# Kernel tuning notes

Hardware: AMD Instinct MI355X
Metric: run time of the kernel (lower is better)

Reference implementation:

```python
import jax, jax.numpy as jnp
import numpy as np

N_NODES = 50000
FEAT_DIM = 256
HIDDEN = 64
CLASS_DIM = 64
N_EDGES = 800000
K_HOPS = 2


def setup_inputs() -> dict:
    key = jax.random.key(0)
    k1, k2, k3, k4, k5, k6 = jax.random.split(key, 6)
    x = jax.random.normal(k1, (N_NODES, FEAT_DIM), dtype=jnp.float32)
    edge_rows = jax.random.randint(k2, (N_EDGES,), 0, N_NODES, dtype=jnp.int32)
    edge_cols = jax.random.randint(k3, (N_EDGES,), 0, N_NODES, dtype=jnp.int32)
    edge_vals = jax.random.uniform(k4, (N_EDGES,), dtype=jnp.float32)  # normalized-adj values (>0)
    # xavier_uniform-style init scale
    lim_e = float(np.sqrt(6.0 / (FEAT_DIM + HIDDEN)))
    lim_c = float(np.sqrt(6.0 / (7 * HIDDEN + CLASS_DIM)))
    w_embed = jax.random.uniform(k5, (FEAT_DIM, HIDDEN), dtype=jnp.float32, minval=-lim_e, maxval=lim_e)
    w_classify = jax.random.uniform(k6, (7 * HIDDEN, CLASS_DIM), dtype=jnp.float32, minval=-lim_c, maxval=lim_c)
    return {"x": x, "edge_rows": edge_rows, "edge_cols": edge_cols,
            "edge_vals": edge_vals, "w_embed": w_embed, "w_classify": w_classify}


def reference(x, edge_rows, edge_cols, edge_vals, w_embed, w_classify):
    # Node_GCN forward (eval mode; dropout inert).
    # a1 = adj - I, a2 = adj@adj - adj - I  =>
    #   a1 @ r = s - r,   a2 @ r = adj@s - s - r   with s = adj @ r
    n = x.shape[0]

    def spmm(r):  # adj @ r via edge-list gather + segment-sum: [n, d]
        return jax.ops.segment_sum(edge_vals[:, None] * r[edge_cols], edge_rows, num_segments=n)

    act = jax.nn.relu
    r = act(x @ w_embed)                  # [n, h]
    rs = [r]
    for _ in range(K_HOPS):
        s = spmm(r)                       # adj @ r
        t = spmm(s)                       # adj @ adj @ r
        r1 = s - r                        # a1 @ r
        r2 = t - s - r                    # a2 @ r
        r = act(jnp.concatenate([r1, r2], axis=1))  # width doubles each hop
        rs.append(r)
    r_final = jnp.concatenate(rs, axis=1)  # [n, 7h]
    return jax.nn.softmax(r_final @ w_classify, axis=1)
```

## Files before the change

kernel.cpp:

```cpp
#include <hip/hip_runtime.h>

#define N_NODES 50000
#define NPAD 50048
#define FEAT 256
#define HID 64
#define NEDGE 800000
#define SCAN_CHUNK 2048
#define NB_SCAN 25
#define NB_EDGE 3125
#define NB_GEMM 391

typedef unsigned short bf16_t;
typedef __attribute__((ext_vector_type(8))) short bf16x8;
typedef __attribute__((ext_vector_type(4))) float f32x4;

#define MFMA_BF16 __builtin_amdgcn_mfma_f32_16x16x32_bf16

__device__ __forceinline__ float bf2f(bf16_t b) {
    union { unsigned u; float f; } v; v.u = ((unsigned)b) << 16; return v.f;
}
__device__ __forceinline__ bf16_t f2bf(float f) {
    union { float f; unsigned u; } v; v.f = f;
    unsigned r = v.u + 0x7fff + ((v.u >> 16) & 1);
    return (bf16_t)(r >> 16);
}
__device__ __forceinline__ void unpack2(unsigned u, float& lo, float& hi) {
    union { unsigned u; float f; } a, b;
    a.u = u << 16; b.u = u & 0xffff0000u;
    lo = a.f; hi = b.f;
}
__device__ __forceinline__ unsigned pack2(float lo, float hi) {
    return ((unsigned)f2bf(lo)) | (((unsigned)f2bf(hi)) << 16);
}

__device__ __forceinline__ void pack_w_body(const float* __restrict__ wsrc,
        bf16_t* __restrict__ wdst, int idx) {
    int lane = idx & 63, nt = (idx >> 6) & 3, ks = idx >> 8;
    int kb  = ks * 32 + ((lane >> 4) * 8);
    int col = nt * 16 + (lane & 15);
    unsigned p[4];
#pragma unroll
    for (int j = 0; j < 4; ++j)
        p[j] = pack2(wsrc[(size_t)(kb + 2*j) * 64 + col],
                     wsrc[(size_t)(kb + 2*j + 1) * 64 + col]);
    uint4 u; u.x = p[0]; u.y = p[1]; u.z = p[2]; u.w = p[3];
    *(uint4*)(wdst + (size_t)idx * 8) = u;
}

__global__ __launch_bounds__(256) void prep_kernel(const int* __restrict__ rows,
        int* __restrict__ cnt, const float* __restrict__ we, bf16_t* __restrict__ wep,
        const float* __restrict__ wc, bf16_t* __restrict__ wcp) {
    const int b = blockIdx.x, t = threadIdx.x;
    if (b < NB_EDGE) {
        int e = b * 256 + t;
        if (e < NEDGE) atomicAdd(&cnt[rows[e]], 1);
    } else if (b < NB_EDGE + 8) {
        pack_w_body(we, wep, (b - NB_EDGE) * 256 + t);
    } else {
        pack_w_body(wc, wcp, (b - NB_EDGE - 8) * 256 + t);
    }
}

__global__ __launch_bounds__(256) void scan_a(const int* __restrict__ cnt,
        int* __restrict__ bsum) {
    __shared__ int sd[256];
    const int t = threadIdx.x;
    const int base = blockIdx.x * SCAN_CHUNK + t * 8;
    int s = 0;
#pragma unroll
    for (int i = 0; i < 8; ++i) {
        int idx = base + i;
        s += (idx < N_NODES) ? cnt[idx] : 0;
    }
    sd[t] = s; __syncthreads();
    for (int off = 128; off > 0; off >>= 1) {
        if (t < off) sd[t] += sd[t + off];
        __syncthreads();
    }
    if (t == 0) bsum[blockIdx.x] = sd[0];
}

__global__ __launch_bounds__(256) void scan_c(const int* __restrict__ cnt,
        const int* __restrict__ bsum, int* __restrict__ rowPtr,
        int* __restrict__ fill) {
    __shared__ int sd[256];
    __shared__ int sboff;
    const int t = threadIdx.x;
    const int base = blockIdx.x * SCAN_CHUNK + t * 8;
    if (t == 0) {
        int a = 0, tot = 0;
        for (int b = 0; b < NB_SCAN; ++b) {
            int v = bsum[b];
            if (b < (int)blockIdx.x) a += v;
            tot += v;
        }
        sboff = a;
        if (blockIdx.x == NB_SCAN - 1) rowPtr[N_NODES] = tot;
    }
    int v[8];
    int s = 0;
#pragma unroll
    for (int i = 0; i < 8; ++i) {
        int idx = base + i;
        v[i] = (idx < N_NODES) ? cnt[idx] : 0;
        s += v[i];
    }
    sd[t] = s; __syncthreads();
    for (int off = 1; off < 256; off <<= 1) {
        int add = (t >= off) ? sd[t - off] : 0;
        __syncthreads();
        sd[t] += add;
        __syncthreads();
    }
    int run = sboff + (sd[t] - s);
#pragma unroll
    for (int i = 0; i < 8; ++i) {
        int idx = base + i;
        if (idx < N_NODES) { rowPtr[idx] = run; fill[idx] = 0; }
        run += v[i];
    }
}

__global__ __launch_bounds__(256) void scatter_embed_kernel(
        const int* __restrict__ rows, const int* __restrict__ cols,
        const float* __restrict__ vals, const int* __restrict__ rowPtr,
        int* __restrict__ fill, uint2* __restrict__ colval,
        const float* __restrict__ x, const bf16_t* __restrict__ wep,
        bf16_t* __restrict__ r0) {
    if (blockIdx.x < NB_EDGE) {
        int e = blockIdx.x * 256 + threadIdx.x;
        if (e < NEDGE) {
            int r = rows[e];
            int p = rowPtr[r] + atomicAdd(&fill[r], 1);
            uint2 cv; cv.x = (unsigned)cols[e]; cv.y = __float_as_uint(vals[e]);
            colval[p] = cv;
        }
        return;
    }
    const int blk = blockIdx.x - NB_EDGE;
    const int t = threadIdx.x;
    const int l = t & 63, w = t >> 6;
    const int lm = l & 15, lg = l >> 4;
    const int base = blk * 128 + w * 32;

    int m0 = base + lm, m1 = base + 16 + lm;
    if (m0 >= N_NODES) m0 = N_NODES - 1;
    if (m1 >= N_NODES) m1 = N_NODES - 1;
    const float* xp0 = x + (size_t)m0 * FEAT + lg * 8;
    const float* xp1 = x + (size_t)m1 * FEAT + lg * 8;

    f32x4 acc[2][4];
#pragma unroll
    for (int i = 0; i < 2; ++i)
#pragma unroll
        for (int j = 0; j < 4; ++j) acc[i][j] = (f32x4){0.f, 0.f, 0.f, 0.f};

    auto aload = [&](const float* p) {
        float4 u0 = *(const float4*)(p);
        float4 u1 = *(const float4*)(p + 4);
        bf16x8 r;
        r[0] = (short)f2bf(u0.x); r[1] = (short)f2bf(u0.y);
        r[2] = (short)f2bf(u0.z); r[3] = (short)f2bf(u0.w);
        r[4] = (short)f2bf(u1.x); r[5] = (short)f2bf(u1.y);
        r[6] = (short)f2bf(u1.z); r[7] = (short)f2bf(u1.w);
        return r;
    };
    auto wb = [&](int ks, int nt) {
        return *(const bf16x8*)(wep + ((size_t)(ks * 4 + nt) * 64 + l) * 8);
    };

    const int NK = FEAT / 32;
    bf16x8 a0 = aload(xp0), a1 = aload(xp1);
    bf16x8 b0 = wb(0,0), b1 = wb(0,1), b2 = wb(0,2), b3 = wb(0,3);
    for (int ks = 0; ks < NK; ++ks) {
        bf16x8 na0, na1, nb0, nb1, nb2, nb3;
        const bool more = (ks + 1 < NK);
        if (more) {
            int kt = (ks + 1) * 32;
            na0 = aload(xp0 + kt); na1 = aload(xp1 + kt);
            nb0 = wb(ks+1,0); nb1 = wb(ks+1,1); nb2 = wb(ks+1,2); nb3 = wb(ks+1,3);
        }
        acc[0][0] = MFMA_BF16(a0, b0, acc[0][0], 0, 0, 0);
        acc[1][0] = MFMA_BF16(a1, b0, acc[1][0], 0, 0, 0);
        acc[0][1] = MFMA_BF16(a0, b1, acc[0][1], 0, 0, 0);
        acc[1][1] = MFMA_BF16(a1, b1, acc[1][1], 0, 0, 0);
        acc[0][2] = MFMA_BF16(a0, b2, acc[0][2], 0, 0, 0);
        acc[1][2] = MFMA_BF16(a1, b2, acc[1][2], 0, 0, 0);
        acc[0][3] = MFMA_BF16(a0, b3, acc[0][3], 0, 0, 0);
        acc[1][3] = MFMA_BF16(a1, b3, acc[1][3], 0, 0, 0);
        if (more) { a0 = na0; a1 = na1; b0 = nb0; b1 = nb1; b2 = nb2; b3 = nb3; }
    }

#pragma unroll
    for (int rt = 0; rt < 2; ++rt)
#pragma unroll
        for (int r = 0; r < 4; ++r) {
            int R = base + rt * 16 + lg * 4 + r;
            if (R < N_NODES) {
                bf16_t* o = r0 + (size_t)R * HID + lm;
                o[0]  = f2bf(fmaxf(acc[rt][0][r], 0.f));
                o[16] = f2bf(fmaxf(acc[rt][1][r], 0.f));
                o[32] = f2bf(fmaxf(acc[rt][2][r], 0.f));
                o[48] = f2bf(fmaxf(acc[rt][3][r], 0.f));
            }
        }
}

__global__ __launch_bounds__(256) void spmm64_kernel(const uint2* __restrict__ colval,
        const int* __restrict__ rowPtr,
        const bf16_t* __restrict__ src, bf16_t* __restrict__ dst) {
    const int lane = threadIdx.x & 63;
    const int row  = (int)((blockIdx.x * 256u + threadIdx.x) >> 6);
    const int beg = rowPtr[row], end = rowPtr[row + 1];
    float acc = 0.f;
    int i = beg;
    for (; i + 8 <= end; i += 8) {
        uint2 cv[8]; float g[8];
#pragma unroll
        for (int j = 0; j < 8; ++j) cv[j] = colval[i+j];
#pragma unroll
        for (int j = 0; j < 8; ++j) g[j] = bf2f(src[(size_t)cv[j].x*HID + lane]);
#pragma unroll
        for (int j = 0; j < 8; ++j) acc += __uint_as_float(cv[j].y)*g[j];
    }
    for (; i < end; ++i) {
        uint2 cv = colval[i];
        acc += __uint_as_float(cv.y) * bf2f(src[(size_t)cv.x*HID + lane]);
    }
    dst[(size_t)row*HID + lane] = f2bf(acc);
}

__global__ __launch_bounds__(256) void spmm64f_kernel(const uint2* __restrict__ colval,
        const int* __restrict__ rowPtr,
        const bf16_t* __restrict__ s, const bf16_t* __restrict__ r0,
        bf16_t* __restrict__ r1c) {
    const int lane = threadIdx.x & 63;
    const int row  = (int)((blockIdx.x * 256u + threadIdx.x) >> 6);
    const int beg = rowPtr[row], end = rowPtr[row + 1];
    float acc = 0.f;
    int i = beg;
    for (; i + 8 <= end; i += 8) {
        uint2 cv[8]; float g[8];
#pragma unroll
        for (int j = 0; j < 8; ++j) cv[j] = colval[i+j];
#pragma unroll
        for (int j = 0; j < 8; ++j) g[j] = bf2f(s[(size_t)cv[j].x*HID + lane]);
#pragma unroll
        for (int j = 0; j < 8; ++j) acc += __uint_as_float(cv[j].y)*g[j];
    }
    for (; i < end; ++i) {
        uint2 cv = colval[i];
        acc += __uint_as_float(cv.y) * bf2f(s[(size_t)cv.x*HID + lane]);
    }
    float sv = bf2f(s[(size_t)row*HID + lane]);
    float rv = bf2f(r0[(size_t)row*HID + lane]);
    r1c[(size_t)row*128 + lane]      = f2bf(fmaxf(sv - rv, 0.f));
    r1c[(size_t)row*128 + 64 + lane] = f2bf(fmaxf(acc - sv - rv, 0.f));
}

__global__ __launch_bounds__(256) void spmm128_kernel(const uint2* __restrict__ colval,
        const int* __restrict__ rowPtr,
        const bf16_t* __restrict__ src, bf16_t* __restrict__ dst) {
    const int lane = threadIdx.x & 63;
    const int row  = (int)((blockIdx.x * 256u + threadIdx.x) >> 6);
    const int beg = rowPtr[row], end = rowPtr[row + 1];
    const unsigned* srcu = (const unsigned*)src;
    float a0 = 0.f, a1 = 0.f;
    int i = beg;
    for (; i + 4 <= end; i += 4) {
        uint2 cv[4]; unsigned u[4];
#pragma unroll
        for (int j = 0; j < 4; ++j) cv[j] = colval[i+j];
#pragma unroll
        for (int j = 0; j < 4; ++j) u[j] = srcu[(size_t)cv[j].x*64 + lane];
#pragma unroll
        for (int j = 0; j < 4; ++j) {
            float lo, hi; unpack2(u[j], lo, hi);
            float v = __uint_as_float(cv[j].y);
            a0 += v*lo; a1 += v*hi;
        }
    }
    for (; i < end; ++i) {
        uint2 cv = colval[i];
        float lo, hi; unpack2(srcu[(size_t)cv.x*64 + lane], lo, hi);
        float v = __uint_as_float(cv.y);
        a0 += v*lo; a1 += v*hi;
    }
    ((unsigned*)dst)[(size_t)row*64 + lane] = pack2(a0, a1);
}

__global__ __launch_bounds__(256) void spmm128f_kernel(const uint2* __restrict__ colval,
        const int* __restrict__ rowPtr,
        const bf16_t* __restrict__ s2, const bf16_t* __restrict__ r1,
        bf16_t* __restrict__ r2c) {
    const int lane = threadIdx.x & 63;
    const int row  = (int)((blockIdx.x * 256u + threadIdx.x) >> 6);
    const int beg = rowPtr[row], end = rowPtr[row + 1];
    const unsigned* s2u = (const unsigned*)s2;
    const unsigned* r1u = (const unsigned*)r1;
    float a0 = 0.f, a1 = 0.f;
    int i = beg;
    for (; i + 4 <= end; i += 4) {
        uint2 cv[4]; unsigned u[4];
#pragma unroll
        for (int j = 0; j < 4; ++j) cv[j] = colval[i+j];
#pragma unroll
        for (int j = 0; j < 4; ++j) u[j] = s2u[(size_t)cv[j].x*64 + lane];
#pragma unroll
        for (int j = 0; j < 4; ++j) {
            float lo, hi; unpack2(u[j], lo, hi);
            float v = __uint_as_float(cv[j].y);
            a0 += v*lo; a1 += v*hi;
        }
    }
    for (; i < end; ++i) {
        uint2 cv = colval[i];
        float lo, hi; unpack2(s2u[(size_t)cv.x*64 + lane], lo, hi);
        float v = __uint_as_float(cv.y);
        a0 += v*lo; a1 += v*hi;
    }
    float s0v, s1v, r0v, r1v;
    unpack2(s2u[(size_t)row*64 + lane], s0v, s1v);
    unpack2(r1u[(size_t)row*64 + lane], r0v, r1v);
    unsigned* r2u = (unsigned*)r2c;
    r2u[(size_t)row*128 + lane]      = pack2(fmaxf(s0v - r0v, 0.f), fmaxf(s1v - r1v, 0.f));
    r2u[(size_t)row*128 + 64 + lane] = pack2(fmaxf(a0 - s0v - r0v, 0.f), fmaxf(a1 - s1v - r1v, 0.f));
}

__global__ __launch_bounds__(256) void classify_mfma(const bf16_t* __restrict__ r0,
        const bf16_t* __restrict__ r1, const bf16_t* __restrict__ r2,
        const bf16_t* __restrict__ wcp, float* __restrict__ out) {
    const int t = threadIdx.x;
    const int l = t & 63, w = t >> 6;
    const int lm = l & 15, lg = l >> 4;
    const int base = blockIdx.x * 128 + w * 32;

    const int m0 = base + lm, m1 = base + 16 + lm;
    const bf16_t* p0_r0 = r0 + (size_t)m0 * 64  + lg * 8;
    const bf16_t* p0_r1 = r1 + (size_t)m0 * 128 + lg * 8;
    const bf16_t* p0_r2 = r2 + (size_t)m0 * 256 + lg * 8;
    const bf16_t* p1_r0 = r0 + (size_t)m1 * 64  + lg * 8;
    const bf16_t* p1_r1 = r1 + (size_t)m1 * 128 + lg * 8;
    const bf16_t* p1_r2 = r2 + (size_t)m1 * 256 + lg * 8;

    f32x4 acc[2][4];
#pragma unroll
    for (int i = 0; i < 2; ++i)
#pragma unroll
        for (int j = 0; j < 4; ++j) acc[i][j] = (f32x4){0.f, 0.f, 0.f, 0.f};

    auto aload = [&](const bf16_t* pr0, const bf16_t* pr1, const bf16_t* pr2, int kt) {
        const bf16_t* p = (kt < 64) ? (pr0 + kt) : (kt < 192) ? (pr1 + kt - 64) : (pr2 + kt - 192);
        return *(const bf16x8*)p;
    };
    auto wb = [&](int ks, int nt) {
        return *(const bf16x8*)(wcp + ((size_t)(ks * 4 + nt) * 64 + l) * 8);
    };

    const int NK = 14;
    bf16x8 a0 = aload(p0_r0, p0_r1, p0_r2, 0);
    bf16x8 a1 = aload(p1_r0, p1_r1, p1_r2, 0);
    bf16x8 b0 = wb(0,0), b1 = wb(0,1), b2 = wb(0,2), b3 = wb(0,3);
    for (int ks = 0; ks < NK; ++ks) {
        bf16x8 na0, na1, nb0, nb1, nb2, nb3;
        const bool more = (ks + 1 < NK);
        if (more) {
            int kt = (ks + 1) * 32;
            na0 = aload(p0_r0, p0_r1, p0_r2, kt);
            na1 = aload(p1_r0, p1_r1, p1_r2, kt);
            nb0 = wb(ks+1,0); nb1 = wb(ks+1,1); nb2 = wb(ks+1,2); nb3 = wb(ks+1,3);
        }
        acc[0][0] = MFMA_BF16(a0, b0, acc[0][0], 0, 0, 0);
        acc[1][0] = MFMA_BF16(a1, b0, acc[1][0], 0, 0, 0);
        acc[0][1] = MFMA_BF16(a0, b1, acc[0][1], 0, 0, 0);
        acc[1][1] = MFMA_BF16(a1, b1, acc[1][1], 0, 0, 0);
        acc[0][2] = MFMA_BF16(a0, b2, acc[0][2], 0, 0, 0);
        acc[1][2] = MFMA_BF16(a1, b2, acc[1][2], 0, 0, 0);
        acc[0][3] = MFMA_BF16(a0, b3, acc[0][3], 0, 0, 0);
        acc[1][3] = MFMA_BF16(a1, b3, acc[1][3], 0, 0, 0);
        if (more) { a0 = na0; a1 = na1; b0 = nb0; b1 = nb1; b2 = nb2; b3 = nb3; }
    }

#pragma unroll
    for (int rt = 0; rt < 2; ++rt)
#pragma unroll
        for (int r = 0; r < 4; ++r) {
            float v0 = acc[rt][0][r], v1 = acc[rt][1][r];
            float v2 = acc[rt][2][r], v3 = acc[rt][3][r];
            float m = fmaxf(fmaxf(v0, v1), fmaxf(v2, v3));
#pragma unroll
            for (int o = 1; o < 16; o <<= 1) m = fmaxf(m, __shfl_xor(m, o));
            float e0 = __expf(v0 - m), e1 = __expf(v1 - m);
            float e2 = __expf(v2 - m), e3 = __expf(v3 - m);
            float s = e0 + e1 + e2 + e3;
#pragma unroll
            for (int o = 1; o < 16; o <<= 1) s += __shfl_xor(s, o);
            float inv = 1.f / s;
            int R = base + rt * 16 + lg * 4 + r;
            if (R < N_NODES) {
                float* o = out + (size_t)R * 64 + lm;
                o[0]  = e0 * inv;
                o[16] = e1 * inv;
                o[32] = e2 * inv;
                o[48] = e3 * inv;
            }
        }
}

extern "C" void kernel_launch(void* const* d_in, const int* in_sizes, int n_in,
                              void* d_out, int out_size, void* d_ws, size_t ws_size,
                              hipStream_t stream) {
    const float* x    = (const float*)d_in[0];
    const int*   erow = (const int*)d_in[1];
    const int*   ecol = (const int*)d_in[2];
    const float* eval = (const float*)d_in[3];
    const float* we   = (const float*)d_in[4];
    const float* wc   = (const float*)d_in[5];
    float* out = (float*)d_out;

    char* wsp = (char*)d_ws;
    size_t off = 0;
    auto take = [&](size_t bytes) {
        char* p = wsp + off;
        off += (bytes + 255) & ~(size_t)255;
        return p;
    };
    bf16_t* r0     = (bf16_t*)take((size_t)NPAD * 64 * 2);
    bf16_t* sbuf   = (bf16_t*)take((size_t)NPAD * 128 * 2);
    bf16_t* r1c    = (bf16_t*)take((size_t)NPAD * 128 * 2);
    bf16_t* r2c    = (bf16_t*)take((size_t)NPAD * 256 * 2);
    int*    cnt    = (int*)take((size_t)N_NODES * 4);
    int*    rowPtr = (int*)take((size_t)(N_NODES + 1) * 4);
    int*    fill   = (int*)take((size_t)N_NODES * 4);
    int*    bsum   = (int*)take((size_t)NB_SCAN * 4);
    uint2*  colval = (uint2*)take((size_t)NEDGE * 8);
    bf16_t* wep    = (bf16_t*)take((size_t)8  * 256 * 8 * 2);
    bf16_t* wcp    = (bf16_t*)take((size_t)14 * 256 * 8 * 2);
    (void)ws_size; (void)in_sizes; (void)n_in; (void)out_size;

    hipMemsetAsync(cnt, 0, (size_t)N_NODES * 4, stream);

    prep_kernel<<<NB_EDGE + 8 + 14, 256, 0, stream>>>(erow, cnt, we, wep, wc, wcp);
    scan_a<<<NB_SCAN, 256, 0, stream>>>(cnt, bsum);
    scan_c<<<NB_SCAN, 256, 0, stream>>>(cnt, bsum, rowPtr, fill);
    scatter_embed_kernel<<<NB_EDGE + NB_GEMM, 256, 0, stream>>>(
        erow, ecol, eval, rowPtr, fill, colval, x, wep, r0);

    spmm64_kernel <<<12500, 256, 0, stream>>>(colval, rowPtr, r0, sbuf);
    spmm64f_kernel<<<12500, 256, 0, stream>>>(colval, rowPtr, sbuf, r0, r1c);
    spmm128_kernel<<<12500, 256, 0, stream>>>(colval, rowPtr, r1c, sbuf);
    spmm128f_kernel<<<12500, 256, 0, stream>>>(colval, rowPtr, sbuf, r1c, r2c);

    classify_mfma<<<NB_GEMM, 256, 0, stream>>>(r0, r1c, r2c, wcp, out);
}
```

Baseline: 274.4 us.

## Store node features in FP8 e4m3 and classify with FP8 MFMA

Switches all intermediate node feature buffers (r0, s, r1, r2) from bf16 to software-encoded fp8 e4m3. This halves the gather traffic in the four SpMM passes and the A-operand reads in the classifier. The classifier moves from bf16 to fp8 MFMA, using weights pre-scaled per hop (1, 2, 8) to cancel the 0.5 and 0.25 downscaling applied to the hop activations. The cost is much lower precision, which risks accuracy tolerance failures, plus extra ALU work for the manual encode and decode.

```diff
diff --git a/kernel.cpp b/kernel.cpp
--- a/kernel.cpp
+++ b/kernel.cpp
@@ -11,29 +11,45 @@
 #define NB_GEMM 391
 
 typedef unsigned short bf16_t;
+typedef unsigned char fp8_t;
+typedef long long i64;
 typedef __attribute__((ext_vector_type(8))) short bf16x8;
 typedef __attribute__((ext_vector_type(4))) float f32x4;
 
 #define MFMA_BF16 __builtin_amdgcn_mfma_f32_16x16x32_bf16
-
-__device__ __forceinline__ float bf2f(bf16_t b) {
-    union { unsigned u; float f; } v; v.u = ((unsigned)b) << 16; return v.f;
-}
+#define MFMA_FP8  __builtin_amdgcn_mfma_f32_16x16x32_fp8_fp8
+
 __device__ __forceinline__ bf16_t f2bf(float f) {
     union { float f; unsigned u; } v; v.f = f;
     unsigned r = v.u + 0x7fff + ((v.u >> 16) & 1);
     return (bf16_t)(r >> 16);
 }
-__device__ __forceinline__ void unpack2(unsigned u, float& lo, float& hi) {
-    union { unsigned u; float f; } a, b;
-    a.u = u << 16; b.u = u & 0xffff0000u;
-    lo = a.f; hi = b.f;
-}
 __device__ __forceinline__ unsigned pack2(float lo, float hi) {
     return ((unsigned)f2bf(lo)) | (((unsigned)f2bf(hi)) << 16);
 }
 
-__device__ __forceinline__ void pack_w_body(const float* __restrict__ wsrc,
+__device__ __forceinline__ unsigned f2e4m3(float f) {
+    union { float f; unsigned u; } v; v.f = f;
+    unsigned s = (v.u >> 24) & 0x80u;
+    unsigned au = v.u & 0x7fffffffu;
+    if (au >= 0x43e80000u) return s | 0x7eu;
+    if (au <  0x3c800000u) return s;
+    unsigned t = au - (120u << 23);
+    t = t + 0x7ffffu + ((t >> 20) & 1u);
+    unsigned w = t >> 20;
+    if (w > 0x7eu) w = 0x7eu;
+    return s | w;
+}
+__device__ __forceinline__ float e4m3f(unsigned b) {
+    unsigned em = b & 0x7fu;
+    unsigned s = (b & 0x80u) << 24;
+    union { unsigned u; float f; } v;
+    if ((em >> 3) == 0) { v.u = s; return v.f; }
+    v.u = s | ((em << 20) + (120u << 23));
+    return v.f;
+}
+
+__device__ __forceinline__ void pack_we_body(const float* __restrict__ wsrc,
         bf16_t* __restrict__ wdst, int idx) {
     int lane = idx & 63, nt = (idx >> 6) & 3, ks = idx >> 8;
     int kb  = ks * 32 + ((lane >> 4) * 8);
@@ -47,17 +63,30 @@
     *(uint4*)(wdst + (size_t)idx * 8) = u;
 }
 
+__device__ __forceinline__ void pack_wc8_body(const float* __restrict__ wsrc,
+        fp8_t* __restrict__ wdst, int idx) {
+    int lane = idx & 63, nt = (idx >> 6) & 3, ks = idx >> 8;
+    int kb  = ks * 32 + ((lane >> 4) * 8);
+    int col = nt * 16 + (lane & 15);
+    float scale = (kb < 64) ? 1.f : (kb < 192) ? 2.f : 8.f;
+    unsigned long long u = 0;
+#pragma unroll
+    for (int j = 0; j < 8; ++j)
+        u |= ((unsigned long long)f2e4m3(wsrc[(size_t)(kb + j) * 64 + col] * scale)) << (8*j);
+    *(unsigned long long*)(wdst + (size_t)idx * 8) = u;
+}
+
 __global__ __launch_bounds__(256) void prep_kernel(const int* __restrict__ rows,
         int* __restrict__ cnt, const float* __restrict__ we, bf16_t* __restrict__ wep,
-        const float* __restrict__ wc, bf16_t* __restrict__ wcp) {
+        const float* __restrict__ wc, fp8_t* __restrict__ wcp) {
     const int b = blockIdx.x, t = threadIdx.x;
     if (b < NB_EDGE) {
         int e = b * 256 + t;
         if (e < NEDGE) atomicAdd(&cnt[rows[e]], 1);
     } else if (b < NB_EDGE + 8) {
-        pack_w_body(we, wep, (b - NB_EDGE) * 256 + t);
+        pack_we_body(we, wep, (b - NB_EDGE) * 256 + t);
     } else {
-        pack_w_body(wc, wcp, (b - NB_EDGE - 8) * 256 + t);
+        pack_wc8_body(wc, wcp, (b - NB_EDGE - 8) * 256 + t);
     }
 }
 
@@ -126,7 +155,7 @@
         const float* __restrict__ vals, const int* __restrict__ rowPtr,
         int* __restrict__ fill, uint2* __restrict__ colval,
         const float* __restrict__ x, const bf16_t* __restrict__ wep,
-        bf16_t* __restrict__ r0) {
+        fp8_t* __restrict__ r0) {
     if (blockIdx.x < NB_EDGE) {
         int e = blockIdx.x * 256 + threadIdx.x;
         if (e < NEDGE) {
@@ -197,18 +226,18 @@
         for (int r = 0; r < 4; ++r) {
             int R = base + rt * 16 + lg * 4 + r;
             if (R < N_NODES) {
-                bf16_t* o = r0 + (size_t)R * HID + lm;
-                o[0]  = f2bf(fmaxf(acc[rt][0][r], 0.f));
-                o[16] = f2bf(fmaxf(acc[rt][1][r], 0.f));
-                o[32] = f2bf(fmaxf(acc[rt][2][r], 0.f));
-                o[48] = f2bf(fmaxf(acc[rt][3][r], 0.f));
+                fp8_t* o = r0 + (size_t)R * HID + lm;
+                o[0]  = (fp8_t)f2e4m3(fmaxf(acc[rt][0][r], 0.f));
+                o[16] = (fp8_t)f2e4m3(fmaxf(acc[rt][1][r], 0.f));
+                o[32] = (fp8_t)f2e4m3(fmaxf(acc[rt][2][r], 0.f));
+                o[48] = (fp8_t)f2e4m3(fmaxf(acc[rt][3][r], 0.f));
             }
         }
 }
 
 __global__ __launch_bounds__(256) void spmm64_kernel(const uint2* __restrict__ colval,
         const int* __restrict__ rowPtr,
-        const bf16_t* __restrict__ src, bf16_t* __restrict__ dst) {
+        const fp8_t* __restrict__ src, fp8_t* __restrict__ dst) {
     const int lane = threadIdx.x & 63;
     const int row  = (int)((blockIdx.x * 256u + threadIdx.x) >> 6);
     const int beg = rowPtr[row], end = rowPtr[row + 1];
@@ -219,21 +248,21 @@
 #pragma unroll
         for (int j = 0; j < 8; ++j) cv[j] = colval[i+j];
 #pragma unroll
-        for (int j = 0; j < 8; ++j) g[j] = bf2f(src[(size_t)cv[j].x*HID + lane]);
+        for (int j = 0; j < 8; ++j) g[j] = e4m3f(src[(size_t)cv[j].x*HID + lane]);
 #pragma unroll
         for (int j = 0; j < 8; ++j) acc += __uint_as_float(cv[j].y)*g[j];
     }
     for (; i < end; ++i) {
         uint2 cv = colval[i];
-        acc += __uint_as_float(cv.y) * bf2f(src[(size_t)cv.x*HID + lane]);
-    }
-    dst[(size_t)row*HID + lane] = f2bf(acc);
+        acc += __uint_as_float(cv.y) * e4m3f(src[(size_t)cv.x*HID + lane]);
+    }
+    dst[(size_t)row*HID + lane] = (fp8_t)f2e4m3(acc);
 }
 
 __global__ __launch_bounds__(256) void spmm64f_kernel(const uint2* __restrict__ colval,
         const int* __restrict__ rowPtr,
-        const bf16_t* __restrict__ s, const bf16_t* __restrict__ r0,
-        bf16_t* __restrict__ r1c) {
+        const fp8_t* __restrict__ s, const fp8_t* __restrict__ r0,
+        fp8_t* __restrict__ r1c) {
     const int lane = threadIdx.x & 63;
     const int row  = (int)((blockIdx.x * 256u + threadIdx.x) >> 6);
     const int beg = rowPtr[row], end = rowPtr[row + 1];
@@ -244,104 +273,112 @@
 #pragma unroll
         for (int j = 0; j < 8; ++j) cv[j] = colval[i+j];
 #pragma unroll
-        for (int j = 0; j < 8; ++j) g[j] = bf2f(s[(size_t)cv[j].x*HID + lane]);
+        for (int j = 0; j < 8; ++j) g[j] = e4m3f(s[(size_t)cv[j].x*HID + lane]);
 #pragma unroll
         for (int j = 0; j < 8; ++j) acc += __uint_as_float(cv[j].y)*g[j];
     }
     for (; i < end; ++i) {
         uint2 cv = colval[i];
-        acc += __uint_as_float(cv.y) * bf2f(s[(size_t)cv.x*HID + lane]);
-    }
-    float sv = bf2f(s[(size_t)row*HID + lane]);
-    float rv = bf2f(r0[(size_t)row*HID + lane]);
-    r1c[(size_t)row*128 + lane]      = f2bf(fmaxf(sv - rv, 0.f));
-    r1c[(size_t)row*128 + 64 + lane] = f2bf(fmaxf(acc - sv - rv, 0.f));
+        acc += __uint_as_float(cv.y) * e4m3f(s[(size_t)cv.x*HID + lane]);
+    }
+    float sv = e4m3f(s[(size_t)row*HID + lane]);
+    float rv = e4m3f(r0[(size_t)row*HID + lane]);
+    r1c[(size_t)row*128 + lane]      = (fp8_t)f2e4m3(0.5f * fmaxf(sv - rv, 0.f));
+    r1c[(size_t)row*128 + 64 + lane] = (fp8_t)f2e4m3(0.5f * fmaxf(acc - sv - rv, 0.f));
 }
 
 __global__ __launch_bounds__(256) void spmm128_kernel(const uint2* __restrict__ colval,
         const int* __restrict__ rowPtr,
-        const bf16_t* __restrict__ src, bf16_t* __restrict__ dst) {
+        const fp8_t* __restrict__ src, fp8_t* __restrict__ dst) {
     const int lane = threadIdx.x & 63;
     const int row  = (int)((blockIdx.x * 256u + threadIdx.x) >> 6);
     const int beg = rowPtr[row], end = rowPtr[row + 1];
-    const unsigned* srcu = (const unsigned*)src;
+    const unsigned short* srcu = (const unsigned short*)src;
     float a0 = 0.f, a1 = 0.f;
     int i = beg;
     for (; i + 4 <= end; i += 4) {
-        uint2 cv[4]; unsigned u[4];
+        uint2 cv[4]; unsigned short u[4];
 #pragma unroll
         for (int j = 0; j < 4; ++j) cv[j] = colval[i+j];
 #pragma unroll
         for (int j = 0; j < 4; ++j) u[j] = srcu[(size_t)cv[j].x*64 + lane];
 #pragma unroll
         for (int j = 0; j < 4; ++j) {
-            float lo, hi; unpack2(u[j], lo, hi);
+            float lo = e4m3f(u[j] & 0xff), hi = e4m3f(u[j] >> 8);
             float v = __uint_as_float(cv[j].y);
             a0 += v*lo; a1 += v*hi;
         }
     }
     for (; i < end; ++i) {
         uint2 cv = colval[i];
-        float lo, hi; unpack2(srcu[(size_t)cv.x*64 + lane], lo, hi);
+        unsigned short u = srcu[(size_t)cv.x*64 + lane];
+        float lo = e4m3f(u & 0xff), hi = e4m3f(u >> 8);
         float v = __uint_as_float(cv.y);
         a0 += v*lo; a1 += v*hi;
     }
-    ((unsigned*)dst)[(size_t)row*64 + lane] = pack2(a0, a1);
+    ((unsigned short*)dst)[(size_t)row*64 + lane] =
+        (unsigned short)(f2e4m3(a0) | (f2e4m3(a1) << 8));
 }
 
 __global__ __launch_bounds__(256) void spmm128f_kernel(const uint2* __restrict__ colval,
         const int* __restrict__ rowPtr,
-        const bf16_t* __restrict__ s2, const bf16_t* __restrict__ r1,
-        bf16_t* __restrict__ r2c) {
+        const fp8_t* __restrict__ s2, const fp8_t* __restrict__ r1,
+        fp8_t* __restrict__ r2c) {
     const int lane = threadIdx.x & 63;
     const int row  = (int)((blockIdx.x * 256u + threadIdx.x) >> 6);
     const int beg = rowPtr[row], end = rowPtr[row + 1];
-    const unsigned* s2u = (const unsigned*)s2;
-    const unsigned* r1u = (const unsigned*)r1;
+    const unsigned short* s2u = (const unsigned short*)s2;
+    const unsigned short* r1u = (const unsigned short*)r1;
     float a0 = 0.f, a1 = 0.f;
     int i = beg;
     for (; i + 4 <= end; i += 4) {
-        uint2 cv[4]; unsigned u[4];
+        uint2 cv[4]; unsigned short u[4];
 #pragma unroll
         for (int j = 0; j < 4; ++j) cv[j] = colval[i+j];
 #pragma unroll
         for (int j = 0; j < 4; ++j) u[j] = s2u[(size_t)cv[j].x*64 + lane];
 #pragma unroll
         for (int j = 0; j < 4; ++j) {
-            float lo, hi; unpack2(u[j], lo, hi);
+            float lo = e4m3f(u[j] & 0xff), hi = e4m3f(u[j] >> 8);
             float v = __uint_as_float(cv[j].y);
             a0 += v*lo; a1 += v*hi;
         }
     }
     for (; i < end; ++i) {
         uint2 cv = colval[i];
-        float lo, hi; unpack2(s2u[(size_t)cv.x*64 + lane], lo, hi);
+        unsigned short u = s2u[(size_t)cv.x*64 + lane];
+        float lo = e4m3f(u & 0xff), hi = e4m3f(u >> 8);
         float v = __uint_as_float(cv.y);
         a0 += v*lo; a1 += v*hi;
     }
-    float s0v, s1v, r0v, r1v;
-    unpack2(s2u[(size_t)row*64 + lane], s0v, s1v);
-    unpack2(r1u[(size_t)row*64 + lane], r0v, r1v);
-    unsigned* r2u = (unsigned*)r2c;
-    r2u[(size_t)row*128 + lane]      = pack2(fmaxf(s0v - r0v, 0.f), fmaxf(s1v - r1v, 0.f));
-    r2u[(size_t)row*128 + 64 + lane] = pack2(fmaxf(a0 - s0v - r0v, 0.f), fmaxf(a1 - s1v - r1v, 0.f));
-}
-
-__global__ __launch_bounds__(256) void classify_mfma(const bf16_t* __restrict__ r0,
-        const bf16_t* __restrict__ r1, const bf16_t* __restrict__ r2,
-        const bf16_t* __restrict__ wcp, float* __restrict__ out) {
+    unsigned short us = s2u[(size_t)row*64 + lane];
+    unsigned short ur = r1u[(size_t)row*64 + lane];
+    float s0v = e4m3f(us & 0xff), s1v = e4m3f(us >> 8);
+    float r0v = e4m3f(ur & 0xff), r1v = e4m3f(ur >> 8);
+    unsigned short* r2u = (unsigned short*)r2c;
+    r2u[(size_t)row*128 + lane] = (unsigned short)(
+        f2e4m3(0.25f * fmaxf(s0v - r0v, 0.f)) |
+        (f2e4m3(0.25f * fmaxf(s1v - r1v, 0.f)) << 8));
+    r2u[(size_t)row*128 + 64 + lane] = (unsigned short)(
+        f2e4m3(0.25f * fmaxf(a0 - s0v - r0v, 0.f)) |
+        (f2e4m3(0.25f * fmaxf(a1 - s1v - r1v, 0.f)) << 8));
+}
+
+__global__ __launch_bounds__(256) void classify_mfma(const fp8_t* __restrict__ r0,
+        const fp8_t* __restrict__ r1, const fp8_t* __restrict__ r2,
+        const fp8_t* __restrict__ wcp, float* __restrict__ out) {
     const int t = threadIdx.x;
     const int l = t & 63, w = t >> 6;
     const int lm = l & 15, lg = l >> 4;
     const int base = blockIdx.x * 128 + w * 32;
 
     const int m0 = base + lm, m1 = base + 16 + lm;
-    const bf16_t* p0_r0 = r0 + (size_t)m0 * 64  + lg * 8;
-    const bf16_t* p0_r1 = r1 + (size_t)m0 * 128 + lg * 8;
-    const bf16_t* p0_r2 = r2 + (size_t)m0 * 256 + lg * 8;
-    const bf16_t* p1_r0 = r0 + (size_t)m1 * 64  + lg * 8;
-    const bf16_t* p1_r1 = r1 + (size_t)m1 * 128 + lg * 8;
-    const bf16_t* p1_r2 = r2 + (size_t)m1 * 256 + lg * 8;
+    const fp8_t* p0_r0 = r0 + (size_t)m0 * 64  + lg * 8;
+    const fp8_t* p0_r1 = r1 + (size_t)m0 * 128 + lg * 8;
+    const fp8_t* p0_r2 = r2 + (size_t)m0 * 256 + lg * 8;
+    const fp8_t* p1_r0 = r0 + (size_t)m1 * 64  + lg * 8;
+    const fp8_t* p1_r1 = r1 + (size_t)m1 * 128 + lg * 8;
+    const fp8_t* p1_r2 = r2 + (size_t)m1 * 256 + lg * 8;
 
     f32x4 acc[2][4];
 #pragma unroll
@@ -349,20 +386,20 @@
 #pragma unroll
         for (int j = 0; j < 4; ++j) acc[i][j] = (f32x4){0.f, 0.f, 0.f, 0.f};
 
-    auto aload = [&](const bf16_t* pr0, const bf16_t* pr1, const bf16_t* pr2, int kt) {
-        const bf16_t* p = (kt < 64) ? (pr0 + kt) : (kt < 192) ? (pr1 + kt - 64) : (pr2 + kt - 192);
-        return *(const bf16x8*)p;
+    auto aload = [&](const fp8_t* pr0, const fp8_t* pr1, const fp8_t* pr2, int kt) {
+        const fp8_t* p = (kt < 64) ? (pr0 + kt) : (kt < 192) ? (pr1 + kt - 64) : (pr2 + kt - 192);
+        return *(const i64*)p;
     };
     auto wb = [&](int ks, int nt) {
-        return *(const bf16x8*)(wcp + ((size_t)(ks * 4 + nt) * 64 + l) * 8);
+        return *(const i64*)(wcp + ((size_t)(ks * 4 + nt) * 64 + l) * 8);
     };
 
     const int NK = 14;
-    bf16x8 a0 = aload(p0_r0, p0_r1, p0_r2, 0);
-    bf16x8 a1 = aload(p1_r0, p1_r1, p1_r2, 0);
-    bf16x8 b0 = wb(0,0), b1 = wb(0,1), b2 = wb(0,2), b3 = wb(0,3);
+    i64 a0 = aload(p0_r0, p0_r1, p0_r2, 0);
+    i64 a1 = aload(p1_r0, p1_r1, p1_r2, 0);
+    i64 b0 = wb(0,0), b1 = wb(0,1), b2 = wb(0,2), b3 = wb(0,3);
     for (int ks = 0; ks < NK; ++ks) {
-        bf16x8 na0, na1, nb0, nb1, nb2, nb3;
+        i64 na0, na1, nb0, nb1, nb2, nb3;
         const bool more = (ks + 1 < NK);
         if (more) {
             int kt = (ks + 1) * 32;
@@ -370,14 +407,14 @@
             na1 = aload(p1_r0, p1_r1, p1_r2, kt);
             nb0 = wb(ks+1,0); nb1 = wb(ks+1,1); nb2 = wb(ks+1,2); nb3 = wb(ks+1,3);
         }
-        acc[0][0] = MFMA_BF16(a0, b0, acc[0][0], 0, 0, 0);
-        acc[1][0] = MFMA_BF16(a1, b0, acc[1][0], 0, 0, 0);
-        acc[0][1] = MFMA_BF16(a0, b1, acc[0][1], 0, 0, 0);
-        acc[1][1] = MFMA_BF16(a1, b1, acc[1][1], 0, 0, 0);
-        acc[0][2] = MFMA_BF16(a0, b2, acc[0][2], 0, 0, 0);
-        acc[1][2] = MFMA_BF16(a1, b2, acc[1][2], 0, 0, 0);
-        acc[0][3] = MFMA_BF16(a0, b3, acc[0][3], 0, 0, 0);
-        acc[1][3] = MFMA_BF16(a1, b3, acc[1][3], 0, 0, 0);
+        acc[0][0] = MFMA_FP8(a0, b0, acc[0][0], 0, 0, 0);
+        acc[1][0] = MFMA_FP8(a1, b0, acc[1][0], 0, 0, 0);
+        acc[0][1] = MFMA_FP8(a0, b1, acc[0][1], 0, 0, 0);
+        acc[1][1] = MFMA_FP8(a1, b1, acc[1][1], 0, 0, 0);
+        acc[0][2] = MFMA_FP8(a0, b2, acc[0][2], 0, 0, 0);
+        acc[1][2] = MFMA_FP8(a1, b2, acc[1][2], 0, 0, 0);
+        acc[0][3] = MFMA_FP8(a0, b3, acc[0][3], 0, 0, 0);
+        acc[1][3] = MFMA_FP8(a1, b3, acc[1][3], 0, 0, 0);
         if (more) { a0 = na0; a1 = na1; b0 = nb0; b1 = nb1; b2 = nb2; b3 = nb3; }
     }
 
@@ -425,17 +462,17 @@
         off += (bytes + 255) & ~(size_t)255;
         return p;
     };
-    bf16_t* r0     = (bf16_t*)take((size_t)NPAD * 64 * 2);
-    bf16_t* sbuf   = (bf16_t*)take((size_t)NPAD * 128 * 2);
-    bf16_t* r1c    = (bf16_t*)take((size_t)NPAD * 128 * 2);
-    bf16_t* r2c    = (bf16_t*)take((size_t)NPAD * 256 * 2);
+    fp8_t*  r0     = (fp8_t*)take((size_t)NPAD * 64);
+    fp8_t*  sbuf   = (fp8_t*)take((size_t)NPAD * 128);
+    fp8_t*  r1c    = (fp8_t*)take((size_t)NPAD * 128);
+    fp8_t*  r2c    = (fp8_t*)take((size_t)NPAD * 256);
     int*    cnt    = (int*)take((size_t)N_NODES * 4);
     int*    rowPtr = (int*)take((size_t)(N_NODES + 1) * 4);
     int*    fill   = (int*)take((size_t)N_NODES * 4);
     int*    bsum   = (int*)take((size_t)NB_SCAN * 4);
     uint2*  colval = (uint2*)take((size_t)NEDGE * 8);
     bf16_t* wep    = (bf16_t*)take((size_t)8  * 256 * 8 * 2);
-    bf16_t* wcp    = (bf16_t*)take((size_t)14 * 256 * 8 * 2);
+    fp8_t*  wcp    = (fp8_t*)take((size_t)14 * 256 * 8);
     (void)ws_size; (void)in_sizes; (void)n_in; (void)out_size;
 
     hipMemsetAsync(cnt, 0, (size_t)N_NODES * 4, stream);
```

After: 299.1 us. 1.09x slower.

## Split 64-wide SpMM wavefronts into half-waves with packed bf16x2 gathers

Applied to the files above, without the earlier changes.

The 64-column SpMM kernels now assign two packed bf16 values per lane. Each half of the wavefront handles alternate edges, and the two partial sums are combined with a cross-half shuffle, so every gather fetches 4-byte words and each wave keeps twice as many edges in flight. The 128-column kernels get their gather unroll raised from 4 to 8 edges for more memory-level parallelism. The cost is extra register pressure, a shuffle reduction per row, and half the lanes sitting idle during the final write.

```diff
diff --git a/kernel.cpp b/kernel.cpp
--- a/kernel.cpp
+++ b/kernel.cpp
@@ -16,9 +16,6 @@
 
 #define MFMA_BF16 __builtin_amdgcn_mfma_f32_16x16x32_bf16
 
-__device__ __forceinline__ float bf2f(bf16_t b) {
-    union { unsigned u; float f; } v; v.u = ((unsigned)b) << 16; return v.f;
-}
 __device__ __forceinline__ bf16_t f2bf(float f) {
     union { float f; unsigned u; } v; v.f = f;
     unsigned r = v.u + 0x7fff + ((v.u >> 16) & 1);
@@ -209,53 +206,91 @@
 __global__ __launch_bounds__(256) void spmm64_kernel(const uint2* __restrict__ colval,
         const int* __restrict__ rowPtr,
         const bf16_t* __restrict__ src, bf16_t* __restrict__ dst) {
-    const int lane = threadIdx.x & 63;
+    const int l = threadIdx.x & 63;
+    const int c = l & 31, h = l >> 5;
     const int row  = (int)((blockIdx.x * 256u + threadIdx.x) >> 6);
     const int beg = rowPtr[row], end = rowPtr[row + 1];
-    float acc = 0.f;
+    const unsigned* srcu = (const unsigned*)src;
+    float a0 = 0.f, a1 = 0.f;
     int i = beg;
-    for (; i + 8 <= end; i += 8) {
-        uint2 cv[8]; float g[8];
-#pragma unroll
-        for (int j = 0; j < 8; ++j) cv[j] = colval[i+j];
-#pragma unroll
-        for (int j = 0; j < 8; ++j) g[j] = bf2f(src[(size_t)cv[j].x*HID + lane]);
-#pragma unroll
-        for (int j = 0; j < 8; ++j) acc += __uint_as_float(cv[j].y)*g[j];
-    }
-    for (; i < end; ++i) {
-        uint2 cv = colval[i];
-        acc += __uint_as_float(cv.y) * bf2f(src[(size_t)cv.x*HID + lane]);
-    }
-    dst[(size_t)row*HID + lane] = f2bf(acc);
+    for (; i + 16 <= end; i += 16) {
+        uint2 cv[8]; unsigned g[8];
+#pragma unroll
+        for (int j = 0; j < 8; ++j) cv[j] = colval[i + 2*j + h];
+#pragma unroll
+        for (int j = 0; j < 8; ++j) g[j] = srcu[(size_t)cv[j].x * 32 + c];
+#pragma unroll
+        for (int j = 0; j < 8; ++j) {
+            float lo, hi; unpack2(g[j], lo, hi);
+            float v = __uint_as_float(cv[j].y);
+            a0 += v*lo; a1 += v*hi;
+        }
+    }
+    for (; i + 2 <= end; i += 2) {
+        uint2 cv = colval[i + h];
+        float lo, hi; unpack2(srcu[(size_t)cv.x*32 + c], lo, hi);
+        float v = __uint_as_float(cv.y);
+        a0 += v*lo; a1 += v*hi;
+    }
+    if (i + h < end) {
+        uint2 cv = colval[i + h];
+        float lo, hi; unpack2(srcu[(size_t)cv.x*32 + c], lo, hi);
+        float v = __uint_as_float(cv.y);
+        a0 += v*lo; a1 += v*hi;
+    }
+    a0 += __shfl_xor(a0, 32);
+    a1 += __shfl_xor(a1, 32);
+    if (h == 0)
+        ((unsigned*)dst)[(size_t)row*32 + c] = pack2(a0, a1);
 }
 
 __global__ __launch_bounds__(256) void spmm64f_kernel(const uint2* __restrict__ colval,
         const int* __restrict__ rowPtr,
         const bf16_t* __restrict__ s, const bf16_t* __restrict__ r0,
         bf16_t* __restrict__ r1c) {
-    const int lane = threadIdx.x & 63;
+    const int l = threadIdx.x & 63;
+    const int c = l & 31, h = l >> 5;
     const int row  = (int)((blockIdx.x * 256u + threadIdx.x) >> 6);
     const int beg = rowPtr[row], end = rowPtr[row + 1];
-    float acc = 0.f;
+    const unsigned* su = (const unsigned*)s;
+    const unsigned* r0u = (const unsigned*)r0;
+    float a0 = 0.f, a1 = 0.f;
     int i = beg;
-    for (; i + 8 <= end; i += 8) {
-        uint2 cv[8]; float g[8];
-#pragma unroll
-        for (int j = 0; j < 8; ++j) cv[j] = colval[i+j];
-#pragma unroll
-        for (int j = 0; j < 8; ++j) g[j] = bf2f(s[(size_t)cv[j].x*HID + lane]);
-#pragma unroll
-        for (int j = 0; j < 8; ++j) acc += __uint_as_float(cv[j].y)*g[j];
-    }
-    for (; i < end; ++i) {
-        uint2 cv = colval[i];
-        acc += __uint_as_float(cv.y) * bf2f(s[(size_t)cv.x*HID + lane]);
-    }
-    float sv = bf2f(s[(size_t)row*HID + lane]);
-    float rv = bf2f(r0[(size_t)row*HID + lane]);
-    r1c[(size_t)row*128 + lane]      = f2bf(fmaxf(sv - rv, 0.f));
-    r1c[(size_t)row*128 + 64 + lane] = f2bf(fmaxf(acc - sv - rv, 0.f));
+    for (; i + 16 <= end; i += 16) {
+        uint2 cv[8]; unsigned g[8];
+#pragma unroll
+        for (int j = 0; j < 8; ++j) cv[j] = colval[i + 2*j + h];
+#pragma unroll
+        for (int j = 0; j < 8; ++j) g[j] = su[(size_t)cv[j].x * 32 + c];
+#pragma unroll
+        for (int j = 0; j < 8; ++j) {
+            float lo, hi; unpack2(g[j], lo, hi);
+            float v = __uint_as_float(cv[j].y);
+            a0 += v*lo; a1 += v*hi;
+        }
+    }
+    for (; i + 2 <= end; i += 2) {
+        uint2 cv = colval[i + h];
+        float lo, hi; unpack2(su[(size_t)cv.x*32 + c], lo, hi);
+        float v = __uint_as_float(cv.y);
+        a0 += v*lo; a1 += v*hi;
+    }
+    if (i + h < end) {
+        uint2 cv = colval[i + h];
+        float lo, hi; unpack2(su[(size_t)cv.x*32 + c], lo, hi);
+        float v = __uint_as_float(cv.y);
+        a0 += v*lo; a1 += v*hi;
+    }
+    a0 += __shfl_xor(a0, 32);
+    a1 += __shfl_xor(a1, 32);
+    if (h == 0) {
+        float sv0, sv1, rv0, rv1;
+        unpack2(su[(size_t)row*32 + c], sv0, sv1);
+        unpack2(r0u[(size_t)row*32 + c], rv0, rv1);
+        unsigned* r1u = (unsigned*)r1c;
+        r1u[(size_t)row*64 + c]      = pack2(fmaxf(sv0 - rv0, 0.f), fmaxf(sv1 - rv1, 0.f));
+        r1u[(size_t)row*64 + 32 + c] = pack2(fmaxf(a0 - sv0 - rv0, 0.f), fmaxf(a1 - sv1 - rv1, 0.f));
+    }
 }
 
 __global__ __launch_bounds__(256) void spmm128_kernel(const uint2* __restrict__ colval,
@@ -267,14 +302,14 @@
     const unsigned* srcu = (const unsigned*)src;
     float a0 = 0.f, a1 = 0.f;
     int i = beg;
-    for (; i + 4 <= end; i += 4) {
-        uint2 cv[4]; unsigned u[4];
-#pragma unroll
-        for (int j = 0; j < 4; ++j) cv[j] = colval[i+j];
-#pragma unroll
-        for (int j = 0; j < 4; ++j) u[j] = srcu[(size_t)cv[j].x*64 + lane];
-#pragma unroll
-        for (int j = 0; j < 4; ++j) {
+    for (; i + 8 <= end; i += 8) {
+        uint2 cv[8]; unsigned u[8];
+#pragma unroll
+        for (int j = 0; j < 8; ++j) cv[j] = colval[i+j];
+#pragma unroll
+        for (int j = 0; j < 8; ++j) u[j] = srcu[(size_t)cv[j].x*64 + lane];
+#pragma unroll
+        for (int j = 0; j < 8; ++j) {
             float lo, hi; unpack2(u[j], lo, hi);
             float v = __uint_as_float(cv[j].y);
             a0 += v*lo; a1 += v*hi;
@@ -300,14 +335,14 @@
     const unsigned* r1u = (const unsigned*)r1;
     float a0 = 0.f, a1 = 0.f;
     int i = beg;
-    for (; i + 4 <= end; i += 4) {
-        uint2 cv[4]; unsigned u[4];
-#pragma unroll
-        for (int j = 0; j < 4; ++j) cv[j] = colval[i+j];
-#pragma unroll
-        for (int j = 0; j < 4; ++j) u[j] = s2u[(size_t)cv[j].x*64 + lane];
-#pragma unroll
-        for (int j = 0; j < 4; ++j) {
+    for (; i + 8 <= end; i += 8) {
+        uint2 cv[8]; unsigned u[8];
+#pragma unroll
+        for (int j = 0; j < 8; ++j) cv[j] = colval[i+j];
+#pragma unroll
+        for (int j = 0; j < 8; ++j) u[j] = s2u[(size_t)cv[j].x*64 + lane];
+#pragma unroll
+        for (int j = 0; j < 8; ++j) {
             float lo, hi; unpack2(u[j], lo, hi);
             float v = __uint_as_float(cv[j].y);
             a0 += v*lo; a1 += v*hi;
```

New measurement: 271.5 us. About the same (-1.1%).
